# Optimization experiments

Hardware: AMD Instinct MI355X
Metric: run time of the kernel (lower is better)

## Reference

```python
import jax, jax.numpy as jnp
import numpy as np

H = 8  # attention heads

def layernorm(x, g, b, eps=1e-6):
    m = x.mean(-1, keepdims=True)
    s = x.std(-1, keepdims=True)
    return g * (x - m) / (s + eps) + b

def mha(qx, kx, vx, mask, W, bv):
    # W: [4,D,D], bv: [4,D]; mask: [B,Lm,Lk] (1=keep) or None
    Bq, Lq, D = qx.shape
    dk = D // H
    def proj(t, i):
        return (t @ W[i] + bv[i]).reshape(t.shape[0], t.shape[1], H, dk).transpose(0, 2, 1, 3)
    q, k, v = proj(qx, 0), proj(kx, 1), proj(vx, 2)
    scores = jnp.einsum('bhqd,bhkd->bhqk', q, k) / np.float32(np.sqrt(dk))
    if mask is not None:
        scores = jnp.where(mask[:, None] == 0, jnp.float32(-1e9), scores)
    a = jax.nn.softmax(scores, axis=-1)
    o = jnp.einsum('bhqk,bhkd->bhqd', a, v).transpose(0, 2, 1, 3).reshape(Bq, Lq, D)
    return o @ W[3] + bv[3]

def ffn(x, w1, b1, w2, b2):
    return jax.nn.relu(x @ w1 + b1) @ w2 + b2

def forward(x, vft, encoded_his, encoded_cap, encoded_query,
            trg_mask, his_mask, cap_mask, query_mask, temporal_mask,
            attn_w, attn_b, ff_w1, ff_b1, ff_w2, ff_b2, ln_g, ln_b):
    B, Ttrg, D = x.shape
    _, T, S, _ = vft.shape
    def sl(i, t, f):  # SublayerConnection: x + f(LayerNorm(x)), dropout=0
        return t + f(layernorm(t, ln_g[i], ln_b[i]))
    s_x = sl(0, x, lambda t: mha(t, t, t, trg_mask, attn_w[0], attn_b[0]))
    h_x = sl(1, s_x, lambda t: mha(t, encoded_his, encoded_his, his_mask, attn_w[1], attn_b[1]))
    c_x = sl(2, h_x, lambda t: mha(t, encoded_cap, encoded_cap, cap_mask, attn_w[2], attn_b[2]))
    mm = sl(3, c_x, lambda t: mha(t, encoded_query, encoded_query, query_mask, attn_w[3], attn_b[3]))
    # --- temporal2spatial: attn over T per spatial location, then attn over S ---
    perm_vft = vft.transpose(0, 2, 1, 3).reshape(B * S, T, D)           # [B*S,T,D]
    exp_in = jnp.broadcast_to(mm[:, None], (B, S, Ttrg, D)).reshape(B * S, Ttrg, D)
    exp_tm = jnp.broadcast_to(temporal_mask[:, None], (B, S, 1, T)).reshape(B * S, 1, T)
    t_out = sl(4, exp_in, lambda t: mha(t, perm_vft, perm_vft, exp_tm, attn_w[4], attn_b[4]))
    p_t = t_out.reshape(B, S, Ttrg, D).transpose(0, 2, 1, 3).reshape(B * Ttrg, S, D)
    unsq = mm.reshape(B * Ttrg, 1, D)
    ts = sl(5, unsq, lambda t: mha(t, p_t, p_t, None, attn_w[5], attn_b[5])).reshape(B, Ttrg, D)
    ts = sl(6, ts, lambda t: ffn(t, ff_w1[0], ff_b1[0], ff_w2[0], ff_b2[0]))
    # --- spatial2temporal: attn over S per frame, then attn over T ---
    rs_vft = vft.reshape(B * T, S, D)                                    # [B*T,S,D]
    exp_in2 = jnp.broadcast_to(mm[:, None], (B, T, Ttrg, D)).reshape(B * T, Ttrg, D)
    s_out = sl(7, exp_in2, lambda t: mha(t, rs_vft, rs_vft, None, attn_w[6], attn_b[6]))
    p_s = s_out.reshape(B, T, Ttrg, D).transpose(0, 2, 1, 3).reshape(B * Ttrg, T, D)
    exp_tm2 = jnp.broadcast_to(temporal_mask[:, None], (B, Ttrg, 1, T)).reshape(B * Ttrg, 1, T)
    st = sl(8, unsq, lambda t: mha(t, p_s, p_s, exp_tm2, attn_w[7], attn_b[7])).reshape(B, Ttrg, D)
    st = sl(9, st, lambda t: ffn(t, ff_w1[1], ff_b1[1], ff_w2[1], ff_b2[1]))
    out = ts + st
    out = sl(10, out, lambda t: ffn(t, ff_w1[2], ff_b1[2], ff_w2[2], ff_b2[2]))
    return out

def setup_inputs() -> dict:
    key = jax.random.key(0)
    ks = jax.random.split(key, 12)
    B, Ttrg, T, S, D, DFF = 16, 64, 64, 49, 512, 2048
    Lhis, Lcap, Lq = 128, 64, 32
    sc = jnp.float32(0.02)
    return {
        'x': jax.random.normal(ks[0], (B, Ttrg, D), jnp.float32),
        'vft': jax.random.normal(ks[1], (B, T, S, D), jnp.float32),
        'encoded_his': jax.random.normal(ks[2], (B, Lhis, D), jnp.float32),
        'encoded_cap': jax.random.normal(ks[3], (B, Lcap, D), jnp.float32),
        'encoded_query': jax.random.normal(ks[4], (B, Lq, D), jnp.float32),
        'trg_mask': jnp.broadcast_to(jnp.tril(jnp.ones((Ttrg, Ttrg), jnp.int32)), (B, Ttrg, Ttrg)),
        'his_mask': jnp.ones((B, 1, Lhis), jnp.int32),
        'cap_mask': jnp.ones((B, 1, Lcap), jnp.int32),
        'query_mask': jnp.ones((B, 1, Lq), jnp.int32),
        'temporal_mask': jnp.ones((B, 1, T), jnp.int32),
        'attn_w': jax.random.normal(ks[5], (8, 4, D, D), jnp.float32) * sc,
        'attn_b': jnp.zeros((8, 4, D), jnp.float32),
        'ff_w1': jax.random.normal(ks[6], (3, D, DFF), jnp.float32) * sc,
        'ff_b1': jnp.zeros((3, DFF), jnp.float32),
        'ff_w2': jax.random.normal(ks[7], (3, DFF, D), jnp.float32) * sc,
        'ff_b2': jnp.zeros((3, D), jnp.float32),
        'ln_g': jnp.ones((11, D), jnp.float32),
        'ln_b': jnp.zeros((11, D), jnp.float32),
    }

def reference(x, vft, encoded_his, encoded_cap, encoded_query,
              trg_mask, his_mask, cap_mask, query_mask, temporal_mask,
              attn_w, attn_b, ff_w1, ff_b1, ff_w2, ff_b2, ln_g, ln_b):
    return forward(x, vft, encoded_his, encoded_cap, encoded_query,
                   trg_mask, his_mask, cap_mask, query_mask, temporal_mask,
                   attn_w, attn_b, ff_w1, ff_b1, ff_w2, ff_b2, ln_g, ln_b)
```

## Files before the change

### kernel.cpp

```cpp
#include <hip/hip_runtime.h>
#include <hip/hip_bf16.h>

typedef unsigned short u16;
typedef short s16x8 __attribute__((ext_vector_type(8)));
typedef unsigned short us8 __attribute__((ext_vector_type(8)));
typedef float f32x4 __attribute__((ext_vector_type(4)));

__device__ __forceinline__ float bf2f(u16 u) {
    unsigned v = ((unsigned)u) << 16;
    float f; __builtin_memcpy(&f, &v, 4); return f;
}
__device__ __forceinline__ u16 f2bf(float f) {
    unsigned v; __builtin_memcpy(&v, &f, 4);
    unsigned r = (v + 0x7FFFu + ((v >> 16) & 1u)) >> 16;
    return (u16)r;
}
__device__ __forceinline__ float4 load4(const float* p) { return *(const float4*)p; }
__device__ __forceinline__ float ld1(const void* p, size_t idx, int isf32) {
    if (isf32) return ((const float*)p)[idx];
    return bf2f(((const u16*)p)[idx]);
}
__device__ __forceinline__ void st1(void* p, size_t idx, float v, int isf32) {
    if (isf32) ((float*)p)[idx] = v;
    else       ((u16*)p)[idx] = f2bf(v);
}
__device__ __forceinline__ void gl16(const u16* gsrc, u16* ldst) {
    __builtin_amdgcn_global_load_lds(
        (const __attribute__((address_space(1))) unsigned int*)gsrc,
        (__attribute__((address_space(3))) unsigned int*)ldst, 16, 0, 0);
}

__global__ __launch_bounds__(256) void detect_k(const unsigned* __restrict__ x, int* __restrict__ flag) {
    __shared__ int cnt_s;
    if (threadIdx.x == 0) cnt_s = 0;
    __syncthreads();
    int c = 0;
    for (int i = threadIdx.x; i < 1024; i += 256) {
        unsigned e = (x[i] >> 23) & 0xFFu;
        if (e >= 110u && e <= 140u) c++;
    }
    #pragma unroll
    for (int off = 32; off; off >>= 1) c += __shfl_xor(c, off);
    if ((threadIdx.x & 63) == 0) atomicAdd(&cnt_s, c);
    __syncthreads();
    if (threadIdx.x == 0) *flag = (cnt_s > 512) ? 1 : 0;
}

__global__ __launch_bounds__(256) void wt_k(const void* __restrict__ W, long in_mstride,
                                            u16* __restrict__ out, long out_mstride,
                                            int K, int N, const int* __restrict__ flag)
{
    __shared__ float t[32][33];
    const int f32 = flag[0];
    const long base = (long)blockIdx.z * in_mstride;
    const int n0 = blockIdx.x << 5, k0 = blockIdx.y << 5;
    const int tx = threadIdx.x & 31, ty = threadIdx.x >> 5;
    #pragma unroll
    for (int i = 0; i < 4; ++i) {
        int kk = ty + (i << 3);
        t[kk][tx] = ld1(W, base + (size_t)(k0 + kk) * N + n0 + tx, f32);
    }
    __syncthreads();
    u16* ob = out + (size_t)blockIdx.z * out_mstride;
    #pragma unroll
    for (int i = 0; i < 4; ++i) {
        int nn = ty + (i << 3);
        ob[(size_t)(n0 + nn) * K + k0 + tx] = f2bf(t[tx][nn]);
    }
}

__global__ __launch_bounds__(256) void cvtb_k(const void* __restrict__ in, u16* __restrict__ out,
                                              long n8, const int* __restrict__ flag)
{
    const int f32 = flag[0];
    const long stride = (long)gridDim.x * 256;
    for (long t = (long)blockIdx.x * 256 + threadIdx.x; t < n8; t += stride) {
        long i = t << 3;
        us8 o;
        if (f32) {
            const float* p = (const float*)in + i;
            float4 a = load4(p), b = load4(p + 4);
            o[0]=f2bf(a.x); o[1]=f2bf(a.y); o[2]=f2bf(a.z); o[3]=f2bf(a.w);
            o[4]=f2bf(b.x); o[5]=f2bf(b.y); o[6]=f2bf(b.z); o[7]=f2bf(b.w);
        } else {
            o = *(const us8*)((const u16*)in + i);
        }
        *(us8*)(out + i) = o;
    }
}

#define LDK 72
__global__ __launch_bounds__(256) void mgemm_k(
    const void* __restrict__ A, long a_off, int a_kind,
    const u16* __restrict__ WT,
    const void* __restrict__ Bv, long b_off,
    const float* __restrict__ R, int rdo, long ros, int rdi, long ris,
    void* __restrict__ C, int c_kind,
    const int* __restrict__ flag,
    int M, int N, int K, int relu)
{
    __shared__ u16 As[64 * LDK];
    __shared__ u16 Ws[64 * LDK];
    const int f32 = flag[0];
    const int af = (a_kind == 0) ? 1 : (a_kind == 1 ? 0 : f32);
    const int cf = (c_kind == 0) ? 1 : (c_kind == 1 ? 0 : f32);
    const int tid = threadIdx.x;
    const int m0 = blockIdx.y << 6, n0 = blockIdx.x << 6;
    const int sr = tid >> 2, sc = (tid & 3) << 4;
    const int wave = tid >> 6, lane = tid & 63;
    const int r0 = (wave & 1) << 5, c0 = (wave >> 1) << 5;
    const int quad = lane >> 4, fl = lane & 15;
    f32x4 acc00 = {0.f,0.f,0.f,0.f}, acc01 = acc00, acc10 = acc00, acc11 = acc00;
    const u16* wrow = WT + (size_t)(n0 + sr) * K;
    for (int k0 = 0; k0 < K; k0 += 64) {
        {
            size_t base = (size_t)a_off + (size_t)(m0 + sr) * K + k0 + sc;
            us8* dst = (us8*)&As[sr * LDK + sc];
            if (af) {
                const float* ap = (const float*)A + base;
                float4 v0 = load4(ap), v1 = load4(ap + 4), v2 = load4(ap + 8), v3 = load4(ap + 12);
                us8 p0, p1;
                p0[0]=f2bf(v0.x); p0[1]=f2bf(v0.y); p0[2]=f2bf(v0.z); p0[3]=f2bf(v0.w);
                p0[4]=f2bf(v1.x); p0[5]=f2bf(v1.y); p0[6]=f2bf(v1.z); p0[7]=f2bf(v1.w);
                p1[0]=f2bf(v2.x); p1[1]=f2bf(v2.y); p1[2]=f2bf(v2.z); p1[3]=f2bf(v2.w);
                p1[4]=f2bf(v3.x); p1[5]=f2bf(v3.y); p1[6]=f2bf(v3.z); p1[7]=f2bf(v3.w);
                dst[0] = p0; dst[1] = p1;
            } else {
                const us8* ap = (const us8*)((const u16*)A + base);
                dst[0] = ap[0]; dst[1] = ap[1];
            }
            const us8* wp = (const us8*)(wrow + k0 + sc);
            us8* wdst = (us8*)&Ws[sr * LDK + sc];
            wdst[0] = wp[0]; wdst[1] = wp[1];
        }
        __syncthreads();
        #pragma unroll
        for (int ks = 0; ks < 2; ++ks) {
            const int kb = (ks << 5) + (quad << 3);
            s16x8 a0 = *(const s16x8*)&As[(r0 + fl) * LDK + kb];
            s16x8 a1 = *(const s16x8*)&As[(r0 + 16 + fl) * LDK + kb];
            s16x8 b0 = *(const s16x8*)&Ws[(c0 + fl) * LDK + kb];
            s16x8 b1 = *(const s16x8*)&Ws[(c0 + 16 + fl) * LDK + kb];
            acc00 = __builtin_amdgcn_mfma_f32_16x16x32_bf16(a0, b0, acc00, 0, 0, 0);
            acc01 = __builtin_amdgcn_mfma_f32_16x16x32_bf16(a0, b1, acc01, 0, 0, 0);
            acc10 = __builtin_amdgcn_mfma_f32_16x16x32_bf16(a1, b0, acc10, 0, 0, 0);
            acc11 = __builtin_amdgcn_mfma_f32_16x16x32_bf16(a1, b1, acc11, 0, 0, 0);
        }
        __syncthreads();
    }
    float bias0 = ld1(Bv, b_off + n0 + c0 + fl, f32);
    float bias1 = ld1(Bv, b_off + n0 + c0 + 16 + fl, f32);
    #pragma unroll
    for (int mt = 0; mt < 2; ++mt) {
        #pragma unroll
        for (int nt = 0; nt < 2; ++nt) {
            f32x4 av = mt ? (nt ? acc11 : acc10) : (nt ? acc01 : acc00);
            float bb = nt ? bias1 : bias0;
            #pragma unroll
            for (int r = 0; r < 4; ++r) {
                int m = m0 + r0 + (mt << 4) + (quad << 2) + r;
                int n = n0 + c0 + (nt << 4) + fl;
                float v = av[r] + bb;
                if (R) v += R[(size_t)(m / rdo) * ros + (size_t)(m % rdi) * ris + n];
                if (relu) v = fmaxf(v, 0.f);
                st1(C, (size_t)m * N + n, v, cf);
            }
        }
    }
}

__global__ __launch_bounds__(256, 4) void bgemm_k(
    const u16* __restrict__ A, long a_off,
    const u16* __restrict__ WT,
    const void* __restrict__ Bv, long b_off,
    const float* __restrict__ R, int rdo, long ros, int rdi, long ris,
    void* __restrict__ C, int c_kind,
    const int* __restrict__ flag,
    int M, int N, int K, int relu)
{
    __shared__ u16 smem[128 * 132];
    u16* As = smem;
    u16* Bs = smem + 128 * 64;
    const int f32 = flag[0];
    const int cf = (c_kind == 0) ? 1 : (c_kind == 1 ? 0 : f32);
    const int tid = threadIdx.x;
    const int gx = gridDim.x;
    int bid = blockIdx.y * gx + blockIdx.x;
    {
        const int nwg = gx * gridDim.y;
        const int q8 = nwg >> 3, r8 = nwg & 7;
        const int xcd = bid & 7, lid = bid >> 3;
        bid = (xcd < r8 ? xcd * (q8 + 1) : r8 * (q8 + 1) + (xcd - r8) * q8) + lid;
    }
    const int m0 = (bid / gx) << 7, n0 = (bid % gx) << 7;
    const int wave = tid >> 6, lane = tid & 63;
    const int r0 = (wave & 1) << 6, c0 = (wave >> 1) << 6;
    const int quad = lane >> 4, fl = lane & 15;
    f32x4 acc[4][4];
    #pragma unroll
    for (int i = 0; i < 4; ++i)
        #pragma unroll
        for (int j = 0; j < 4; ++j) { acc[i][j][0]=0.f; acc[i][j][1]=0.f; acc[i][j][2]=0.f; acc[i][j][3]=0.f; }
    const int rl = (wave << 5) + (lane >> 3);
    const int csw = (((lane & 7) ^ (lane >> 3)) << 3);
    const u16* Ab = A + a_off + (size_t)(m0 + rl) * K + csw;
    const u16* Bb = WT + (size_t)(n0 + rl) * K + csw;
    for (int k0 = 0; k0 < K; k0 += 64) {
        #pragma unroll
        for (int s = 0; s < 4; ++s) {
            gl16(Ab + (size_t)(s << 3) * K + k0, &As[((wave << 5) + (s << 3)) << 6]);
            gl16(Bb + (size_t)(s << 3) * K + k0, &Bs[((wave << 5) + (s << 3)) << 6]);
        }
        __syncthreads();
        #pragma unroll
        for (int ks = 0; ks < 2; ++ks) {
            const int ac = ((ks << 5) + (quad << 3)) ^ ((fl & 7) << 3);
            s16x8 a[4], b[4];
            #pragma unroll
            for (int i = 0; i < 4; ++i) {
                a[i] = *(const s16x8*)&As[((r0 + (i << 4) + fl) << 6) + ac];
                b[i] = *(const s16x8*)&Bs[((c0 + (i << 4) + fl) << 6) + ac];
            }
            #pragma unroll
            for (int i = 0; i < 4; ++i)
                #pragma unroll
                for (int j = 0; j < 4; ++j)
                    acc[i][j] = __builtin_amdgcn_mfma_f32_16x16x32_bf16(a[i], b[j], acc[i][j], 0, 0, 0);
        }
        __syncthreads();
    }
    if (cf == 0) {
        #pragma unroll
        for (int j = 0; j < 4; ++j) {
            float bb = ld1(Bv, b_off + n0 + c0 + (j << 4) + fl, f32);
            #pragma unroll
            for (int i = 0; i < 4; ++i) {
                #pragma unroll
                for (int r = 0; r < 4; ++r) {
                    int lm = r0 + (i << 4) + (quad << 2) + r;
                    int m = m0 + lm;
                    float v = 0.f;
                    if (m < M) {
                        v = acc[i][j][r] + bb;
                        if (R) v += R[(size_t)(m / rdo) * ros + (size_t)(m % rdi) * ris + (n0 + c0 + (j << 4) + fl)];
                        if (relu) v = fmaxf(v, 0.f);
                    }
                    smem[lm * 132 + c0 + (j << 4) + fl] = f2bf(v);
                }
            }
        }
        __syncthreads();
        u16* Cb = (u16*)C + n0;
        #pragma unroll
        for (int it = 0; it < 8; ++it) {
            int idx = it * 256 + tid;
            int row = idx >> 4, ch = (idx & 15) << 3;
            if (m0 + row < M)
                *(us8*)(Cb + (size_t)(m0 + row) * N + ch) = *(const us8*)&smem[row * 132 + ch];
        }
    } else {
        #pragma unroll
        for (int j = 0; j < 4; ++j) {
            float bb = ld1(Bv, b_off + n0 + c0 + (j << 4) + fl, f32);
            #pragma unroll
            for (int i = 0; i < 4; ++i) {
                #pragma unroll
                for (int r = 0; r < 4; ++r) {
                    int m = m0 + r0 + (i << 4) + (quad << 2) + r;
                    if (m < M) {
                        int n = n0 + c0 + (j << 4) + fl;
                        float v = acc[i][j][r] + bb;
                        if (R) v += R[(size_t)(m / rdo) * ros + (size_t)(m % rdi) * ris + n];
                        if (relu) v = fmaxf(v, 0.f);
                        ((float*)C)[(size_t)m * N + n] = v;
                    }
                }
            }
        }
    }
}

__global__ __launch_bounds__(256, 4) void pgemm_k(
    const u16* __restrict__ A, long a_off,
    const u16* __restrict__ WTq, const u16* __restrict__ WTr,
    const void* __restrict__ Bv, long boff1, long boff2,
    u16* __restrict__ C1, u16* __restrict__ C2,
    const int* __restrict__ flag, int M)
{
    __shared__ u16 smem[128 * 132];
    u16* As = smem;
    u16* Bs = smem + 128 * 64;
    const int f32 = flag[0];
    const int tid = threadIdx.x;
    int bid = blockIdx.y * 16 + blockIdx.x;
    {
        const int nwg = 16 * gridDim.y;
        const int q8 = nwg >> 3, r8 = nwg & 7;
        const int xcd = bid & 7, lid = bid >> 3;
        bid = (xcd < r8 ? xcd * (q8 + 1) : r8 * (q8 + 1) + (xcd - r8) * q8) + lid;
    }
    const int m0 = (bid >> 4) << 7, n0 = (bid & 15) << 7;
    const int wave = tid >> 6, lane = tid & 63;
    const int r0 = (wave & 1) << 6, c0 = (wave >> 1) << 6;
    const int quad = lane >> 4, fl = lane & 15;
    f32x4 acc[4][4];
    #pragma unroll
    for (int i = 0; i < 4; ++i)
        #pragma unroll
        for (int j = 0; j < 4; ++j) { acc[i][j][0]=0.f; acc[i][j][1]=0.f; acc[i][j][2]=0.f; acc[i][j][3]=0.f; }
    const int rl = (wave << 5) + (lane >> 3);
    const int csw = (((lane & 7) ^ (lane >> 3)) << 3);
    const u16* Ab = A + a_off + (size_t)(m0 + rl) * 512 + csw;
    const u16* WTp = (n0 < 1024) ? WTq + (size_t)n0 * 512 : WTr + (size_t)(n0 - 1024) * 512;
    const u16* Bb = WTp + (size_t)rl * 512 + csw;
    for (int k0 = 0; k0 < 512; k0 += 64) {
        #pragma unroll
        for (int s = 0; s < 4; ++s) {
            gl16(Ab + (size_t)(s << 3) * 512 + k0, &As[((wave << 5) + (s << 3)) << 6]);
            gl16(Bb + (size_t)(s << 3) * 512 + k0, &Bs[((wave << 5) + (s << 3)) << 6]);
        }
        __syncthreads();
        #pragma unroll
        for (int ks = 0; ks < 2; ++ks) {
            const int ac = ((ks << 5) + (quad << 3)) ^ ((fl & 7) << 3);
            s16x8 a[4], b[4];
            #pragma unroll
            for (int i = 0; i < 4; ++i) {
                a[i] = *(const s16x8*)&As[((r0 + (i << 4) + fl) << 6) + ac];
                b[i] = *(const s16x8*)&Bs[((c0 + (i << 4) + fl) << 6) + ac];
            }
            #pragma unroll
            for (int i = 0; i < 4; ++i)
                #pragma unroll
                for (int j = 0; j < 4; ++j)
                    acc[i][j] = __builtin_amdgcn_mfma_f32_16x16x32_bf16(a[i], b[j], acc[i][j], 0, 0, 0);
        }
        __syncthreads();
    }
    const int half2 = (n0 >= 1024);
    const long boff = half2 ? (boff2 + n0 - 1024) : (boff1 + n0);
    #pragma unroll
    for (int j = 0; j < 4; ++j) {
        float bb = ld1(Bv, boff + c0 + (j << 4) + fl, f32);
        #pragma unroll
        for (int i = 0; i < 4; ++i) {
            #pragma unroll
            for (int r = 0; r < 4; ++r) {
                int lm = r0 + (i << 4) + (quad << 2) + r;
                smem[lm * 132 + c0 + (j << 4) + fl] = f2bf(acc[i][j][r] + bb);
            }
        }
    }
    __syncthreads();
    u16* Cb = half2 ? (C2 + (n0 - 1024)) : (C1 + n0);
    #pragma unroll
    for (int it = 0; it < 8; ++it) {
        int idx = it * 256 + tid;
        int row = idx >> 4, ch = (idx & 15) << 3;
        if (m0 + row < M)
            *(us8*)(Cb + (size_t)(m0 + row) * 1024 + ch) = *(const us8*)&smem[row * 132 + ch];
    }
}

#define ALD 72
__global__ __launch_bounds__(256) void mattn_k(
    const u16* __restrict__ Q, long z_q, long q_g, long q_r,
    const u16* __restrict__ Kp, long z_k, long k_g, long k_r,
    const u16* __restrict__ Vp, long z_v, long v_g, long v_r,
    u16* __restrict__ O, long z_o, long o_g, long o_r,
    const int* __restrict__ mask, long z_m, long m_g, int m_perq,
    int Lq, int Lk, float scale)
{
    extern __shared__ u16 sm[];
    u16* Ks  = sm;
    u16* VsT = sm + 64 * ALD;
    u16* Ps  = sm + 128 * ALD;
    const int h = blockIdx.x, g = blockIdx.y, z = blockIdx.z;
    const int tid = threadIdx.x, wave = tid >> 6, lane = tid & 63;
    const int quad = lane >> 4, fl = lane & 15;
    const u16* kb = Kp + (long)z * z_k + (long)g * k_g + h * 64;
    const u16* vb = Vp + (long)z * z_v + (long)g * v_g + h * 64;
    for (int idx = tid; idx < 512; idx += 256) {
        int ki = idx >> 3, c = (idx & 7) << 3;
        us8 kv = {0,0,0,0,0,0,0,0}, vv = kv;
        if (ki < Lk) {
            kv = *(const us8*)&kb[(long)ki * k_r + c];
            vv = *(const us8*)&vb[(long)ki * v_r + c];
        }
        *(us8*)&Ks[ki * ALD + c] = kv;
        #pragma unroll
        for (int j = 0; j < 8; ++j) VsT[(c + j) * ALD + ki] = vv[j];
    }
    __syncthreads();
    const int q0 = wave << 4;
    s16x8 aq0 = {0,0,0,0,0,0,0,0}, aq1 = aq0;
    {
        int qi = q0 + fl;
        if (qi < Lq) {
            const u16* qp = Q + (long)z * z_q + (long)g * q_g + (long)qi * q_r + h * 64 + (quad << 3);
            aq0 = *(const s16x8*)qp;
            aq1 = *(const s16x8*)(qp + 32);
        }
    }
    f32x4 S[4];
    __builtin_amdgcn_s_setprio(1);
    #pragma unroll
    for (int nt = 0; nt < 4; ++nt) {
        const u16* krow = &Ks[((nt << 4) + fl) * ALD + (quad << 3)];
        s16x8 b0 = *(const s16x8*)krow;
        s16x8 b1 = *(const s16x8*)(krow + 32);
        f32x4 acc = {0.f, 0.f, 0.f, 0.f};
        acc = __builtin_amdgcn_mfma_f32_16x16x32_bf16(aq0, b0, acc, 0, 0, 0);
        acc = __builtin_amdgcn_mfma_f32_16x16x32_bf16(aq1, b1, acc, 0, 0, 0);
        S[nt] = acc;
    }
    __builtin_amdgcn_s_setprio(0);
    const int* mb = mask ? mask + (long)z * z_m + (long)g * m_g : nullptr;
    #pragma unroll
    for (int nt = 0; nt < 4; ++nt) {
        int key = (nt << 4) + fl;
        if (key >= Lk) {
            S[nt][0] = S[nt][1] = S[nt][2] = S[nt][3] = -3.0e38f;
        } else if (mb && !m_perq) {
            float pen = (mb[key] == 0) ? -1e9f : 0.f;
            #pragma unroll
            for (int r = 0; r < 4; ++r) S[nt][r] = S[nt][r] * scale + pen;
        } else if (mb) {
            #pragma unroll
            for (int r = 0; r < 4; ++r) {
                int q = q0 + (quad << 2) + r;
                float v = S[nt][r] * scale;
                if (mb[(long)q * Lk + key] == 0) v = -1e9f;
                S[nt][r] = v;
            }
        } else {
            #pragma unroll
            for (int r = 0; r < 4; ++r) S[nt][r] *= scale;
        }
    }
    #pragma unroll
    for (int r = 0; r < 4; ++r) {
        float m = fmaxf(fmaxf(S[0][r], S[1][r]), fmaxf(S[2][r], S[3][r]));
        m = fmaxf(m, __shfl_xor(m, 1)); m = fmaxf(m, __shfl_xor(m, 2));
        m = fmaxf(m, __shfl_xor(m, 4)); m = fmaxf(m, __shfl_xor(m, 8));
        float sum = 0.f;
        #pragma unroll
        for (int nt = 0; nt < 4; ++nt) { float e = __expf(S[nt][r] - m); S[nt][r] = e; sum += e; }
        sum += __shfl_xor(sum, 1); sum += __shfl_xor(sum, 2);
        sum += __shfl_xor(sum, 4); sum += __shfl_xor(sum, 8);
        float inv = 1.f / sum;
        #pragma unroll
        for (int nt = 0; nt < 4; ++nt) S[nt][r] *= inv;
    }
    {
        u16* pw = Ps + (size_t)(wave << 4) * ALD;
        #pragma unroll
        for (int nt = 0; nt < 4; ++nt) {
            int key = (nt << 4) + fl;
            #pragma unroll
            for (int r = 0; r < 4; ++r)
                pw[((quad << 2) + r) * ALD + key] = f2bf(S[nt][r]);
        }
    }
    __syncthreads();
    const u16* prow = &Ps[(size_t)((wave << 4) + fl) * ALD + (quad << 3)];
    s16x8 ap0 = *(const s16x8*)prow;
    s16x8 ap1 = *(const s16x8*)(prow + 32);
    #pragma unroll
    for (int nt = 0; nt < 4; ++nt) {
        const u16* vrow = &VsT[((nt << 4) + fl) * ALD + (quad << 3)];
        s16x8 b0 = *(const s16x8*)vrow;
        s16x8 b1 = *(const s16x8*)(vrow + 32);
        f32x4 acc = {0.f, 0.f, 0.f, 0.f};
        __builtin_amdgcn_s_setprio(1);
        acc = __builtin_amdgcn_mfma_f32_16x16x32_bf16(ap0, b0, acc, 0, 0, 0);
        acc = __builtin_amdgcn_mfma_f32_16x16x32_bf16(ap1, b1, acc, 0, 0, 0);
        __builtin_amdgcn_s_setprio(0);
        #pragma unroll
        for (int r = 0; r < 4; ++r) {
            int q = q0 + (quad << 2) + r;
            if (q < Lq)
                O[(long)z * z_o + (long)g * o_g + (long)q * o_r + h * 64 + (nt << 4) + fl] = f2bf(acc[r]);
        }
    }
}

__global__ __launch_bounds__(256) void mattn128_k(
    const u16* __restrict__ Q, long z_q, long q_g, long q_r,
    const u16* __restrict__ Kp, long z_k, long k_g, long k_r,
    const u16* __restrict__ Vp, long z_v, long v_g, long v_r,
    u16* __restrict__ O, long z_o, long o_g, long o_r,
    const int* __restrict__ mask, long z_m, long m_g,
    float scale)
{
    extern __shared__ u16 sm[];
    u16* Ks  = sm;
    u16* VsT = sm + 128 * 72;
    u16* Ps  = sm + 128 * 72 + 64 * 136;
    const int h = blockIdx.x, g = blockIdx.y, z = blockIdx.z;
    const int tid = threadIdx.x, wave = tid >> 6, lane = tid & 63;
    const int quad = lane >> 4, fl = lane & 15;
    const u16* kb = Kp + (long)z * z_k + (long)g * k_g + h * 64;
    const u16* vb = Vp + (long)z * z_v + (long)g * v_g + h * 64;
    for (int idx = tid; idx < 1024; idx += 256) {
        int ki = idx >> 3, c = (idx & 7) << 3;
        *(us8*)&Ks[ki * 72 + c] = *(const us8*)&kb[(long)ki * k_r + c];
        us8 v = *(const us8*)&vb[(long)ki * v_r + c];
        #pragma unroll
        for (int j = 0; j < 8; ++j) VsT[(c + j) * 136 + ki] = v[j];
    }
    __syncthreads();
    const int q0 = wave << 4;
    s16x8 aq0, aq1;
    {
        const u16* qp = Q + (long)z * z_q + (long)g * q_g + (long)(q0 + fl) * q_r + h * 64 + (quad << 3);
        aq0 = *(const s16x8*)qp;
        aq1 = *(const s16x8*)(qp + 32);
    }
    f32x4 S[8];
    __builtin_amdgcn_s_setprio(1);
    #pragma unroll
    for (int nt = 0; nt < 8; ++nt) {
        const u16* krow = &Ks[((nt << 4) + fl) * 72 + (quad << 3)];
        s16x8 b0 = *(const s16x8*)krow;
        s16x8 b1 = *(const s16x8*)(krow + 32);
        f32x4 acc = {0.f, 0.f, 0.f, 0.f};
        acc = __builtin_amdgcn_mfma_f32_16x16x32_bf16(aq0, b0, acc, 0, 0, 0);
        acc = __builtin_amdgcn_mfma_f32_16x16x32_bf16(aq1, b1, acc, 0, 0, 0);
        S[nt] = acc;
    }
    __builtin_amdgcn_s_setprio(0);
    const int* mb = mask ? mask + (long)z * z_m + (long)g * m_g : nullptr;
    #pragma unroll
    for (int nt = 0; nt < 8; ++nt) {
        int key = (nt << 4) + fl;
        float pen = (mb && mb[key] == 0) ? -1e9f : 0.f;
        #pragma unroll
        for (int r = 0; r < 4; ++r) S[nt][r] = S[nt][r] * scale + pen;
    }
    #pragma unroll
    for (int r = 0; r < 4; ++r) {
        float m = S[0][r];
        #pragma unroll
        for (int nt = 1; nt < 8; ++nt) m = fmaxf(m, S[nt][r]);
        m = fmaxf(m, __shfl_xor(m, 1)); m = fmaxf(m, __shfl_xor(m, 2));
        m = fmaxf(m, __shfl_xor(m, 4)); m = fmaxf(m, __shfl_xor(m, 8));
        float sum = 0.f;
        #pragma unroll
        for (int nt = 0; nt < 8; ++nt) { float e = __expf(S[nt][r] - m); S[nt][r] = e; sum += e; }
        sum += __shfl_xor(sum, 1); sum += __shfl_xor(sum, 2);
        sum += __shfl_xor(sum, 4); sum += __shfl_xor(sum, 8);
        float inv = 1.f / sum;
        #pragma unroll
        for (int nt = 0; nt < 8; ++nt) S[nt][r] *= inv;
    }
    {
        u16* pw = Ps + (size_t)q0 * 136;
        #pragma unroll
        for (int nt = 0; nt < 8; ++nt) {
            int key = (nt << 4) + fl;
            #pragma unroll
            for (int r = 0; r < 4; ++r)
                pw[((quad << 2) + r) * 136 + key] = f2bf(S[nt][r]);
        }
    }
    __syncthreads();
    const u16* prow = &Ps[(size_t)(q0 + fl) * 136];
    s16x8 ap[4];
    #pragma unroll
    for (int kc = 0; kc < 4; ++kc) ap[kc] = *(const s16x8*)&prow[(kc << 5) + (quad << 3)];
    #pragma unroll
    for (int nt = 0; nt < 4; ++nt) {
        const u16* vrow = &VsT[((nt << 4) + fl) * 136];
        f32x4 acc = {0.f, 0.f, 0.f, 0.f};
        __builtin_amdgcn_s_setprio(1);
        #pragma unroll
        for (int kc = 0; kc < 4; ++kc) {
            s16x8 b = *(const s16x8*)&vrow[(kc << 5) + (quad << 3)];
            acc = __builtin_amdgcn_mfma_f32_16x16x32_bf16(ap[kc], b, acc, 0, 0, 0);
        }
        __builtin_amdgcn_s_setprio(0);
        #pragma unroll
        for (int r = 0; r < 4; ++r) {
            int q = q0 + (quad << 2) + r;
            O[(long)z * z_o + (long)g * o_g + (long)q * o_r + h * 64 + (nt << 4) + fl] = f2bf(acc[r]);
        }
    }
}

__global__ __launch_bounds__(512) void attn1_k(
    const u16* __restrict__ Q, long z_q, long q_g,
    const u16* __restrict__ Kp, long z_k, long k_g, long k_r,
    const u16* __restrict__ Vp, long z_v, long v_g, long v_r,
    u16* __restrict__ O, long z_o, long o_g,
    const int* __restrict__ mask, long z_m,
    int Lk, float scale)
{
    const int g = blockIdx.x, z = blockIdx.y;
    const int h = threadIdx.x >> 6, lane = threadIdx.x & 63;
    const float ql = bf2f(Q[(long)z * z_q + (long)g * q_g + (h << 6) + lane]);
    const int kid = (lane < Lk) ? lane : 0;
    const u16* krow = Kp + (long)z * z_k + (long)g * k_g + (long)kid * k_r + (h << 6);
    s16x8 kv[8];
    #pragma unroll
    for (int i = 0; i < 8; ++i) kv[i] = ((const s16x8*)krow)[i];
    float acc = 0.f;
    #pragma unroll
    for (int i = 0; i < 8; ++i) {
        #pragma unroll
        for (int j = 0; j < 8; ++j)
            acc += __shfl(ql, (i << 3) + j) * bf2f((u16)kv[i][j]);
    }
    float s = (lane < Lk) ? acc * scale : -3.0e38f;
    if (mask && lane < Lk && mask[(long)z * z_m + lane] == 0) s = -1e9f;
    float mx = s;
    #pragma unroll
    for (int off = 32; off; off >>= 1) mx = fmaxf(mx, __shfl_xor(mx, off));
    float e = __expf(s - mx);
    float sum = e;
    #pragma unroll
    for (int off = 32; off; off >>= 1) sum += __shfl_xor(sum, off);
    const float a = e * (1.f / sum);
    const u16* vbase = Vp + (long)z * z_v + (long)g * v_g + (h << 6) + lane;
    float o = 0.f;
    #pragma unroll 8
    for (int ki = 0; ki < Lk; ++ki)
        o += __shfl(a, ki) * bf2f(vbase[(long)ki * v_r]);
    O[(long)z * z_o + (long)g * o_g + (h << 6) + lane] = f2bf(o);
}

__global__ __launch_bounds__(256) void ln_k(const float* __restrict__ X, u16* __restrict__ Y,
                                            const void* __restrict__ g, const void* __restrict__ b,
                                            long p_off, const int* __restrict__ flag)
{
    const int f32 = flag[0];
    const int row = blockIdx.x, tid = threadIdx.x;
    const float* x = X + (size_t)row * 512;
    float x0 = x[tid], x1 = x[tid + 256];
    float s = x0 + x1, ss = x0 * x0 + x1 * x1;
    #pragma unroll
    for (int off = 32; off; off >>= 1) { s += __shfl_xor(s, off); ss += __shfl_xor(ss, off); }
    __shared__ float rs[4], rss[4];
    int wave = tid >> 6, lane = tid & 63;
    if (lane == 0) { rs[wave] = s; rss[wave] = ss; }
    __syncthreads();
    s = rs[0] + rs[1] + rs[2] + rs[3];
    ss = rss[0] + rss[1] + rss[2] + rss[3];
    float mean = s * (1.f / 512.f);
    float var = fmaxf(ss * (1.f / 512.f) - mean * mean, 0.f);
    float inv = 1.f / (sqrtf(var) + 1e-6f);
    u16* y = Y + (size_t)row * 512;
    y[tid]       = f2bf(ld1(g, p_off + tid, f32)       * (x0 - mean) * inv + ld1(b, p_off + tid, f32));
    y[tid + 256] = f2bf(ld1(g, p_off + tid + 256, f32) * (x1 - mean) * inv + ld1(b, p_off + tid + 256, f32));
}

__global__ __launch_bounds__(256) void ln2_k(const float* __restrict__ Xa, const float* __restrict__ Xb,
                                             float* __restrict__ Sfull, u16* __restrict__ Y,
                                             const void* __restrict__ g, const void* __restrict__ b,
                                             long p_off, const int* __restrict__ flag)
{
    const int f32 = flag[0];
    const int row = blockIdx.x, tid = threadIdx.x;
    const size_t base = (size_t)row * 512;
    float x0 = Xa[base + tid] + Xb[base + tid];
    float x1 = Xa[base + tid + 256] + Xb[base + tid + 256];
    Sfull[base + tid] = x0;
    Sfull[base + tid + 256] = x1;
    float s = x0 + x1, ss = x0 * x0 + x1 * x1;
    #pragma unroll
    for (int off = 32; off; off >>= 1) { s += __shfl_xor(s, off); ss += __shfl_xor(ss, off); }
    __shared__ float rs[4], rss[4];
    int wave = tid >> 6, lane = tid & 63;
    if (lane == 0) { rs[wave] = s; rss[wave] = ss; }
    __syncthreads();
    s = rs[0] + rs[1] + rs[2] + rs[3];
    ss = rss[0] + rss[1] + rss[2] + rss[3];
    float mean = s * (1.f / 512.f);
    float var = fmaxf(ss * (1.f / 512.f) - mean * mean, 0.f);
    float inv = 1.f / (sqrtf(var) + 1e-6f);
    u16* y = Y + base;
    y[tid]       = f2bf(ld1(g, p_off + tid, f32)       * (x0 - mean) * inv + ld1(b, p_off + tid, f32));
    y[tid + 256] = f2bf(ld1(g, p_off + tid + 256, f32) * (x1 - mean) * inv + ld1(b, p_off + tid + 256, f32));
}

__global__ __launch_bounds__(256) void cvt_k(const void* __restrict__ in, float* __restrict__ out,
                                             int n, const int* __restrict__ flag) {
    const int f32 = flag[0];
    int i = blockIdx.x * 256 + threadIdx.x;
    if (i < n) out[i] = ld1(in, i, f32);
}

extern "C" void kernel_launch(void* const* d_in, const int* in_sizes, int n_in,
                              void* d_out, int out_size, void* d_ws, size_t ws_size,
                              hipStream_t stream)
{
    const void* x    = d_in[0];
    const void* vft  = d_in[1];
    const void* his  = d_in[2];
    const void* cap  = d_in[3];
    const void* qry  = d_in[4];
    const int* trg_m = (const int*)d_in[5];
    const int* his_m = (const int*)d_in[6];
    const int* cap_m = (const int*)d_in[7];
    const int* qry_m = (const int*)d_in[8];
    const int* tmp_m = (const int*)d_in[9];
    const void* aw  = d_in[10];
    const void* ab  = d_in[11];
    const void* fw1 = d_in[12];
    const void* fb1 = d_in[13];
    const void* fw2 = d_in[14];
    const void* fb2 = d_in[15];
    const void* lng = d_in[16];
    const void* lnb = d_in[17];

    char* wsb = (char*)d_ws;
    size_t off = 0;
    auto alloc = [&](size_t bytes) {
        void* p = wsb + off; off += (bytes + 131072 + 255) & ~(size_t)255; return p;
    };
    int*   FLAG = (int*)alloc(256);
    float* XF  = (float*)alloc(524288 * 4);
    float* SX  = (float*)alloc(524288 * 4);
    float* HX  = (float*)alloc(524288 * 4);
    float* CX  = (float*)alloc(524288 * 4);
    float* MM  = (float*)alloc(524288 * 4);
    float* TS0 = (float*)alloc(524288 * 4);
    float* TS  = (float*)alloc(524288 * 4);
    float* ST0 = (float*)alloc(524288 * 4);
    float* ST  = (float*)alloc(524288 * 4);
    float* O0  = (float*)alloc(524288 * 4);
    u16*   L   = (u16*)alloc(524288 * 2);
    u16*   QA  = (u16*)alloc(524288 * 2);
    u16*   QB  = (u16*)alloc(524288 * 2);
    u16*   QC  = (u16*)alloc(524288 * 2);
    u16*   QD  = (u16*)alloc(524288 * 2);
    u16*   QKV = (u16*)alloc(1572864 * 2);
    u16*   Kb  = (u16*)alloc(2097152 * 2);
    u16*   AO1 = (u16*)alloc(524288 * 2);
    u16*   AO2 = (u16*)alloc(524288 * 2);
    u16*   FB  = (u16*)alloc(2097152 * 2);
    u16*   WTa = (u16*)alloc((size_t)32 * 262144 * 2);
    u16*   WT1 = (u16*)alloc((size_t)3 * 1048576 * 2);
    u16*   WT2 = (u16*)alloc((size_t)3 * 1048576 * 2);
    u16*   VFTB = (u16*)alloc((size_t)25690112 * 2);
    int CH = 1;
    {
        const size_t perCH = ((size_t)6422528 + 1605632 + 2097152 + 2097152) * 2 + 4 * 131584;
        for (int c : {16, 8, 4, 2, 1}) {
            if (off + (size_t)c * perCH <= ws_size) { CH = c; break; }
        }
    }
    u16* KVR  = (u16*)alloc((size_t)CH * 6422528 * 2);
    u16* BAOt = (u16*)alloc((size_t)CH * 1605632 * 2);
    u16* BAOs = (u16*)alloc((size_t)CH * 2097152 * 2);
    u16* BOb  = (u16*)alloc((size_t)CH * 2097152 * 2);
    if (off > ws_size) return;

    detect_k<<<1, 256, 0, stream>>>((const unsigned*)x, FLAG);
    wt_k<<<dim3(16, 16, 32), 256, 0, stream>>>(aw, 262144, WTa, 262144, 512, 512, FLAG);
    wt_k<<<dim3(64, 16, 3),  256, 0, stream>>>(fw1, 1048576, WT1, 1048576, 512, 2048, FLAG);
    wt_k<<<dim3(16, 64, 3),  256, 0, stream>>>(fw2, 1048576, WT2, 1048576, 2048, 512, FLAG);
    cvtb_k<<<2048, 256, 0, stream>>>(vft, VFTB, 3211264, FLAG);

    auto WO  = [&](int l, int j) { return (size_t)(l * 4 + j) * 262144; };
    auto BOf = [&](int l, int j) { return (long)(l * 4 + j) * 512; };

    auto mg = [&](const void* A, long a_off, int a_kind, const u16* WTp, const void* Bvp, long b_off,
                  const float* R, int rdo, long ros, int rdi, long ris,
                  void* C, int c_kind, int M, int N, int K, int relu) {
        int gy = (M + 127) >> 7;
        if (a_kind == 1 && (M & 63) == 0 && (N & 127) == 0 && (K & 63) == 0 && gy * (N >> 7) >= 64)
            bgemm_k<<<dim3(N >> 7, gy), 256, 0, stream>>>((const u16*)A, a_off, WTp, Bvp, b_off,
                                                          R, rdo, ros, rdi, ris, C, c_kind, FLAG, M, N, K, relu);
        else
            mgemm_k<<<dim3(N / 64, M / 64), 256, 0, stream>>>(A, a_off, a_kind, WTp, Bvp, b_off,
                                                              R, rdo, ros, rdi, ris, C, c_kind, FLAG, M, N, K, relu);
    };
    auto mattn = [&](const u16* Q, long zq, long qg, long qr,
                     const u16* K, long zk, long kg, long kr,
                     const u16* V, long zv, long vg, long vr,
                     u16* O, long zo, long og, long orr,
                     const int* mp, long zm, long mg_, int mperq,
                     int nZ, int nG, int Lq, int Lk) {
        size_t smem = (size_t)192 * ALD * 2;
        mattn_k<<<dim3(8, nG, nZ), 256, smem, stream>>>(Q, zq, qg, qr, K, zk, kg, kr, V, zv, vg, vr,
                                                        O, zo, og, orr, mp, zm, mg_, mperq, Lq, Lk, 0.125f);
    };
    auto ln = [&](const float* X, int i) {
        ln_k<<<1024, 256, 0, stream>>>(X, L, lng, lnb, (long)i * 512, FLAG);
    };

    cvt_k<<<2048, 256, 0, stream>>>(x, XF, 524288, FLAG);

    ln(XF, 0);
    mg(L, 0, 1, WTa + WO(0,0), ab, BOf(0,0), nullptr,1,0,1,0, QKV, 1, 1024,1536,512, 0);
    mattn(QKV,0,98304,1536, QKV+512,0,98304,1536, QKV+1024,0,98304,1536,
          AO1,0,32768,512, trg_m,0,4096,1, 1,16,64,64);
    mg(AO1, 0, 1, WTa + WO(0,3), ab, BOf(0,3), XF,1,512,1,0, SX, 0, 1024,512,512, 0);

    ln(SX, 1);
    mg(L, 0, 1, WTa + WO(1,0), ab, BOf(1,0), nullptr,1,0,1,0, QA, 1, 1024,512,512, 0);
    mg(his, 0, 2, WTa + WO(1,1), ab, BOf(1,1), nullptr,1,0,1,0, Kb, 1, 2048,1024,512, 0);
    {
        size_t smem128 = (size_t)(128 * 72 + 2 * 64 * 136) * 2;
        mattn128_k<<<dim3(8, 16, 1), 256, smem128, stream>>>(QA,0,32768,512,
                                                             Kb,0,131072,1024, Kb+512,0,131072,1024,
                                                             AO1,0,32768,512, his_m, 0, 128, 0.125f);
    }
    mg(AO1, 0, 1, WTa + WO(1,3), ab, BOf(1,3), SX,1,512,1,0, HX, 0, 1024,512,512, 0);

    ln(HX, 2);
    mg(L, 0, 1, WTa + WO(2,0), ab, BOf(2,0), nullptr,1,0,1,0, QA, 1, 1024,512,512, 0);
    mg(cap, 0, 2, WTa + WO(2,1), ab, BOf(2,1), nullptr,1,0,1,0, Kb, 1, 1024,1024,512, 0);
    mattn(QA,0,32768,512, Kb,0,65536,1024, Kb+512,0,65536,1024,
          AO1,0,32768,512, cap_m,0,64,0, 1,16,64,64);
    mg(AO1, 0, 1, WTa + WO(2,3), ab, BOf(2,3), HX,1,512,1,0, CX, 0, 1024,512,512, 0);

    ln(CX, 3);
    mg(L, 0, 1, WTa + WO(3,0), ab, BOf(3,0), nullptr,1,0,1,0, QA, 1, 1024,512,512, 0);
    mg(qry, 0, 2, WTa + WO(3,1), ab, BOf(3,1), nullptr,1,0,1,0, Kb, 1, 512,1024,512, 0);
    mattn(QA,0,32768,512, Kb,0,32768,1024, Kb+512,0,32768,1024,
          AO1,0,32768,512, qry_m,0,32,0, 1,16,64,32);
    mg(AO1, 0, 1, WTa + WO(3,3), ab, BOf(3,3), CX,1,512,1,0, MM, 0, 1024,512,512, 0);

    ln(MM, 4); mg(L, 0, 1, WTa + WO(4,0), ab, BOf(4,0), nullptr,1,0,1,0, QA, 1, 1024,512,512, 0);
    ln(MM, 5); mg(L, 0, 1, WTa + WO(5,0), ab, BOf(5,0), nullptr,1,0,1,0, QB, 1, 1024,512,512, 0);
    ln(MM, 7); mg(L, 0, 1, WTa + WO(6,0), ab, BOf(6,0), nullptr,1,0,1,0, QC, 1, 1024,512,512, 0);
    ln(MM, 8); mg(L, 0, 1, WTa + WO(7,0), ab, BOf(7,0), nullptr,1,0,1,0, QD, 1, 1024,512,512, 0);

    u16* C1 = KVR;
    u16* C2 = KVR + (size_t)CH * 3211264;
    for (int cb = 0; cb < 16; cb += CH) {
        long voff = (long)cb * 1605632;
        int Mc1 = CH * 3136, Mc2 = CH * 4096;
        pgemm_k<<<dim3(16, (Mc1 + 127) >> 7), 256, 0, stream>>>(
            VFTB, voff, WTa + WO(4,1), WTa + WO(6,1), ab, BOf(4,1), BOf(6,1), C1, C2, FLAG, Mc1);
        mattn(QA + cb*32768, 32768,0,512, C1,3211264,1024,50176, C1+512,3211264,1024,50176,
              BAOt,1605632,32768,512, tmp_m + cb*64, 64,0,0, CH,49,64,64);
        mattn(QC + cb*32768, 32768,0,512, C2,3211264,50176,1024, C2+512,3211264,50176,1024,
              BAOs,2097152,32768,512, nullptr,0,0,0, CH,64,64,49);
        mg(BAOt, 0, 1, WTa + WO(4,3), ab, BOf(4,3), MM + cb*32768, 3136,32768,64,512, BOb, 1, Mc1,512,512, 0);
        mg(BOb, 0, 1, WTa + WO(5,1), ab, BOf(5,1), nullptr,1,0,1,0, KVR, 1, Mc1,1024,512, 0);
        attn1_k<<<dim3(64, CH), 512, 0, stream>>>(QB + cb*32768, 32768, 512,
                                                  KVR, 3211264, 1024, 65536,
                                                  KVR + 512, 3211264, 1024, 65536,
                                                  AO1 + cb*32768, 32768, 512,
                                                  nullptr, 0, 49, 0.125f);
        mg(BAOs, 0, 1, WTa + WO(6,3), ab, BOf(6,3), MM + cb*32768, 4096,32768,64,512, BOb, 1, Mc2,512,512, 0);
        mg(BOb, 0, 1, WTa + WO(7,1), ab, BOf(7,1), nullptr,1,0,1,0, KVR, 1, Mc2,1024,512, 0);
        attn1_k<<<dim3(64, CH), 512, 0, stream>>>(QD + cb*32768, 32768, 512,
                                                  KVR, 4194304, 1024, 65536,
                                                  KVR + 512, 4194304, 1024, 65536,
                                                  AO2 + cb*32768, 32768, 512,
                                                  tmp_m + cb*64, 64, 64, 0.125f);
    }

    mg(AO1, 0, 1, WTa + WO(5,3), ab, BOf(5,3), MM,1,512,1,0, TS0, 0, 1024,512,512, 0);
    ln(TS0, 6);
    mg(L, 0, 1, WT1 + 0, fb1, 0, nullptr,1,0,1,0, FB, 1, 1024,2048,512, 1);
    mg(FB, 0, 1, WT2 + 0, fb2, 0, TS0,1,512,1,0, TS, 0, 1024,512,2048, 0);

    mg(AO2, 0, 1, WTa + WO(7,3), ab, BOf(7,3), MM,1,512,1,0, ST0, 0, 1024,512,512, 0);
    ln(ST0, 9);
    mg(L, 0, 1, WT1 + 1048576, fb1, 2048, nullptr,1,0,1,0, FB, 1, 1024,2048,512, 1);
    mg(FB, 0, 1, WT2 + 1048576, fb2, 512, ST0,1,512,1,0, ST, 0, 1024,512,2048, 0);

    ln2_k<<<1024, 256, 0, stream>>>(TS, ST, O0, L, lng, lnb, (long)10 * 512, FLAG);
    mg(L, 0, 1, WT1 + 2097152, fb1, 4096, nullptr,1,0,1,0, FB, 1, 1024,2048,512, 1);
    mg(FB, 0, 1, WT2 + 2097152, fb2, 1024, O0,1,512,1,0, d_out, 2, 1024,512,2048, 0);
}
```

Baseline: 1.456 ms.

## Fold output projection into next K/V projection and fuse four layernorms

Precomputes a combined weight for the output projection followed by the next K/V projection (W_o·W_kv), so each chunk runs one GEMM instead of two and skips the intermediate BOb buffer. The residual term (MM plus bias, projected through W_kv) is computed once per token up front and broadcast in as the residual input. The four layernorms on MM are merged into one kernel that computes statistics once and writes four outputs. This reorders and changes the rounding of the arithmetic, since the combined weight is stored in bf16, and it adds setup GEMMs and extra buffers.

```diff
diff --git a/kernel.cpp b/kernel.cpp
--- a/kernel.cpp
+++ b/kernel.cpp
@@ -70,7 +70,7 @@
 }
 
 __global__ __launch_bounds__(256) void cvtb_k(const void* __restrict__ in, u16* __restrict__ out,
-                                              long n8, const int* __restrict__ flag)
+                                              long n8, long off, const int* __restrict__ flag)
 {
     const int f32 = flag[0];
     const long stride = (long)gridDim.x * 256;
@@ -78,15 +78,27 @@
         long i = t << 3;
         us8 o;
         if (f32) {
-            const float* p = (const float*)in + i;
+            const float* p = (const float*)in + off + i;
             float4 a = load4(p), b = load4(p + 4);
             o[0]=f2bf(a.x); o[1]=f2bf(a.y); o[2]=f2bf(a.z); o[3]=f2bf(a.w);
             o[4]=f2bf(b.x); o[5]=f2bf(b.y); o[6]=f2bf(b.z); o[7]=f2bf(b.w);
         } else {
-            o = *(const us8*)((const u16*)in + i);
+            o = *(const us8*)((const u16*)in + off + i);
         }
         *(us8*)(out + i) = o;
     }
+}
+
+__global__ __launch_bounds__(256) void zf_k(float* __restrict__ p, int n) {
+    int i = blockIdx.x * 256 + threadIdx.x;
+    if (i < n) p[i] = 0.f;
+}
+__global__ __launch_bounds__(256) void addb_k(const float* __restrict__ X, float* __restrict__ out,
+                                              const void* __restrict__ bias, long b_off, int n,
+                                              const int* __restrict__ flag) {
+    const int f32 = flag[0];
+    int i = blockIdx.x * 256 + threadIdx.x;
+    if (i < n) out[i] = X[i] + ld1(bias, b_off + (i & 511), f32);
 }
 
 #define LDK 72
@@ -654,6 +666,39 @@
     y[tid + 256] = f2bf(ld1(g, p_off + tid + 256, f32) * (x1 - mean) * inv + ld1(b, p_off + tid + 256, f32));
 }
 
+__global__ __launch_bounds__(256) void ln4_k(const float* __restrict__ X,
+                                             u16* __restrict__ Y0, u16* __restrict__ Y1,
+                                             u16* __restrict__ Y2, u16* __restrict__ Y3,
+                                             const void* __restrict__ g, const void* __restrict__ b,
+                                             const int* __restrict__ flag)
+{
+    const int f32 = flag[0];
+    const int row = blockIdx.x, tid = threadIdx.x;
+    const float* x = X + (size_t)row * 512;
+    float x0 = x[tid], x1 = x[tid + 256];
+    float s = x0 + x1, ss = x0 * x0 + x1 * x1;
+    #pragma unroll
+    for (int off = 32; off; off >>= 1) { s += __shfl_xor(s, off); ss += __shfl_xor(ss, off); }
+    __shared__ float rs[4], rss[4];
+    int wave = tid >> 6, lane = tid & 63;
+    if (lane == 0) { rs[wave] = s; rss[wave] = ss; }
+    __syncthreads();
+    s = rs[0] + rs[1] + rs[2] + rs[3];
+    ss = rss[0] + rss[1] + rss[2] + rss[3];
+    float mean = s * (1.f / 512.f);
+    float var = fmaxf(ss * (1.f / 512.f) - mean * mean, 0.f);
+    float inv = 1.f / (sqrtf(var) + 1e-6f);
+    float n0v = (x0 - mean) * inv, n1v = (x1 - mean) * inv;
+    const size_t base = (size_t)row * 512;
+    u16* Ys[4] = {Y0, Y1, Y2, Y3};
+    const long po[4] = {4*512, 5*512, 7*512, 8*512};
+    #pragma unroll
+    for (int i = 0; i < 4; ++i) {
+        Ys[i][base + tid]       = f2bf(ld1(g, po[i] + tid, f32)       * n0v + ld1(b, po[i] + tid, f32));
+        Ys[i][base + tid + 256] = f2bf(ld1(g, po[i] + tid + 256, f32) * n1v + ld1(b, po[i] + tid + 256, f32));
+    }
+}
+
 __global__ __launch_bounds__(256) void ln2_k(const float* __restrict__ Xa, const float* __restrict__ Xb,
                                              float* __restrict__ Sfull, u16* __restrict__ Y,
                                              const void* __restrict__ g, const void* __restrict__ b,
@@ -730,6 +775,9 @@
     float* ST  = (float*)alloc(524288 * 4);
     float* O0  = (float*)alloc(524288 * 4);
     u16*   L   = (u16*)alloc(524288 * 2);
+    u16*   L5  = (u16*)alloc(524288 * 2);
+    u16*   L7  = (u16*)alloc(524288 * 2);
+    u16*   L8  = (u16*)alloc(524288 * 2);
     u16*   QA  = (u16*)alloc(524288 * 2);
     u16*   QB  = (u16*)alloc(524288 * 2);
     u16*   QC  = (u16*)alloc(524288 * 2);
@@ -743,9 +791,17 @@
     u16*   WT1 = (u16*)alloc((size_t)3 * 1048576 * 2);
     u16*   WT2 = (u16*)alloc((size_t)3 * 1048576 * 2);
     u16*   VFTB = (u16*)alloc((size_t)25690112 * 2);
+    u16*   AWB43 = (u16*)alloc(262144 * 2);
+    u16*   AWB63 = (u16*)alloc(262144 * 2);
+    u16*   WT45  = (u16*)alloc(524288 * 2);
+    u16*   WT67  = (u16*)alloc(524288 * 2);
+    float* ZEROB = (float*)alloc(1024 * 4);
+    float* MMB   = (float*)alloc(524288 * 4);
+    float* MMP1  = (float*)alloc(1048576 * 4);
+    float* MMP2  = (float*)alloc(1048576 * 4);
     int CH = 1;
     {
-        const size_t perCH = ((size_t)6422528 + 1605632 + 2097152 + 2097152) * 2 + 4 * 131584;
+        const size_t perCH = ((size_t)6422528 + 1605632 + 2097152) * 2 + 3 * 131584;
         for (int c : {16, 8, 4, 2, 1}) {
             if (off + (size_t)c * perCH <= ws_size) { CH = c; break; }
         }
@@ -753,14 +809,16 @@
     u16* KVR  = (u16*)alloc((size_t)CH * 6422528 * 2);
     u16* BAOt = (u16*)alloc((size_t)CH * 1605632 * 2);
     u16* BAOs = (u16*)alloc((size_t)CH * 2097152 * 2);
-    u16* BOb  = (u16*)alloc((size_t)CH * 2097152 * 2);
     if (off > ws_size) return;
 
     detect_k<<<1, 256, 0, stream>>>((const unsigned*)x, FLAG);
     wt_k<<<dim3(16, 16, 32), 256, 0, stream>>>(aw, 262144, WTa, 262144, 512, 512, FLAG);
     wt_k<<<dim3(64, 16, 3),  256, 0, stream>>>(fw1, 1048576, WT1, 1048576, 512, 2048, FLAG);
     wt_k<<<dim3(16, 64, 3),  256, 0, stream>>>(fw2, 1048576, WT2, 1048576, 2048, 512, FLAG);
-    cvtb_k<<<2048, 256, 0, stream>>>(vft, VFTB, 3211264, FLAG);
+    cvtb_k<<<2048, 256, 0, stream>>>(vft, VFTB, 3211264, 0, FLAG);
+    cvtb_k<<<128, 256, 0, stream>>>(aw, AWB43, 32768, (long)19 * 262144, FLAG);
+    cvtb_k<<<128, 256, 0, stream>>>(aw, AWB63, 32768, (long)27 * 262144, FLAG);
+    zf_k<<<4, 256, 0, stream>>>(ZEROB, 1024);
 
     auto WO  = [&](int l, int j) { return (size_t)(l * 4 + j) * 262144; };
     auto BOf = [&](int l, int j) { return (long)(l * 4 + j) * 512; };
@@ -790,6 +848,9 @@
         ln_k<<<1024, 256, 0, stream>>>(X, L, lng, lnb, (long)i * 512, FLAG);
     };
 
+    mg(WTa + WO(5,1), 0, 1, AWB43, ZEROB, 0, nullptr,1,0,1,0, WT45, 1, 1024,512,512, 0);
+    mg(WTa + WO(7,1), 0, 1, AWB63, ZEROB, 0, nullptr,1,0,1,0, WT67, 1, 1024,512,512, 0);
+
     cvt_k<<<2048, 256, 0, stream>>>(x, XF, 524288, FLAG);
 
     ln(XF, 0);
@@ -823,10 +884,16 @@
           AO1,0,32768,512, qry_m,0,32,0, 1,16,64,32);
     mg(AO1, 0, 1, WTa + WO(3,3), ab, BOf(3,3), CX,1,512,1,0, MM, 0, 1024,512,512, 0);
 
-    ln(MM, 4); mg(L, 0, 1, WTa + WO(4,0), ab, BOf(4,0), nullptr,1,0,1,0, QA, 1, 1024,512,512, 0);
-    ln(MM, 5); mg(L, 0, 1, WTa + WO(5,0), ab, BOf(5,0), nullptr,1,0,1,0, QB, 1, 1024,512,512, 0);
-    ln(MM, 7); mg(L, 0, 1, WTa + WO(6,0), ab, BOf(6,0), nullptr,1,0,1,0, QC, 1, 1024,512,512, 0);
-    ln(MM, 8); mg(L, 0, 1, WTa + WO(7,0), ab, BOf(7,0), nullptr,1,0,1,0, QD, 1, 1024,512,512, 0);
+    ln4_k<<<1024, 256, 0, stream>>>(MM, L, L5, L7, L8, lng, lnb, FLAG);
+    mg(L,  0, 1, WTa + WO(4,0), ab, BOf(4,0), nullptr,1,0,1,0, QA, 1, 1024,512,512, 0);
+    mg(L5, 0, 1, WTa + WO(5,0), ab, BOf(5,0), nullptr,1,0,1,0, QB, 1, 1024,512,512, 0);
+    mg(L7, 0, 1, WTa + WO(6,0), ab, BOf(6,0), nullptr,1,0,1,0, QC, 1, 1024,512,512, 0);
+    mg(L8, 0, 1, WTa + WO(7,0), ab, BOf(7,0), nullptr,1,0,1,0, QD, 1, 1024,512,512, 0);
+
+    addb_k<<<2048, 256, 0, stream>>>(MM, MMB, ab, BOf(4,3), 524288, FLAG);
+    mg(MMB, 0, 0, WTa + WO(5,1), ab, BOf(5,1), nullptr,1,0,1,0, MMP1, 0, 1024,1024,512, 0);
+    addb_k<<<2048, 256, 0, stream>>>(MM, MMB, ab, BOf(6,3), 524288, FLAG);
+    mg(MMB, 0, 0, WTa + WO(7,1), ab, BOf(7,1), nullptr,1,0,1,0, MMP2, 0, 1024,1024,512, 0);
 
     u16* C1 = KVR;
     u16* C2 = KVR + (size_t)CH * 3211264;
@@ -839,15 +906,15 @@
               BAOt,1605632,32768,512, tmp_m + cb*64, 64,0,0, CH,49,64,64);
         mattn(QC + cb*32768, 32768,0,512, C2,3211264,50176,1024, C2+512,3211264,50176,1024,
               BAOs,2097152,32768,512, nullptr,0,0,0, CH,64,64,49);
-        mg(BAOt, 0, 1, WTa + WO(4,3), ab, BOf(4,3), MM + cb*32768, 3136,32768,64,512, BOb, 1, Mc1,512,512, 0);
-        mg(BOb, 0, 1, WTa + WO(5,1), ab, BOf(5,1), nullptr,1,0,1,0, KVR, 1, Mc1,1024,512, 0);
+        mg(BAOt, 0, 1, WT45, ZEROB, 0, MMP1 + (size_t)cb*65536, 3136,65536,64,1024,
+           KVR, 1, Mc1,1024,512, 0);
         attn1_k<<<dim3(64, CH), 512, 0, stream>>>(QB + cb*32768, 32768, 512,
                                                   KVR, 3211264, 1024, 65536,
                                                   KVR + 512, 3211264, 1024, 65536,
                                                   AO1 + cb*32768, 32768, 512,
                                                   nullptr, 0, 49, 0.125f);
-        mg(BAOs, 0, 1, WTa + WO(6,3), ab, BOf(6,3), MM + cb*32768, 4096,32768,64,512, BOb, 1, Mc2,512,512, 0);
-        mg(BOb, 0, 1, WTa + WO(7,1), ab, BOf(7,1), nullptr,1,0,1,0, KVR, 1, Mc2,1024,512, 0);
+        mg(BAOs, 0, 1, WT67, ZEROB, 0, MMP2 + (size_t)cb*65536, 4096,65536,64,1024,
+           KVR, 1, Mc2,1024,512, 0);
         attn1_k<<<dim3(64, CH), 512, 0, stream>>>(QD + cb*32768, 32768, 512,
                                                   KVR, 4194304, 1024, 65536,
                                                   KVR + 512, 4194304, 1024, 65536,
```

After: 1.459 ms. About the same (+0.2%).
